# Performance work log

Measured on AMD Instinct MI355X. Metric: run time of the kernel, lower is better.

## Reference

```python
import jax, jax.numpy as jnp
import numpy as np

ATOM_F = 64
NBR_F = 64
IN_F = 2 * ATOM_F + NBR_F  # 192
ATTN = ATOM_F              # 64
ATTN_OUT = 4 * ATOM_F      # 256
EPS = 1e-5


def setup_inputs() -> dict:
    key = jax.random.key(0)
    ks = jax.random.split(key, 12)
    N, M = 65536, 12
    atom_in_fea = jax.random.normal(ks[0], (N, ATOM_F), dtype=jnp.float32)
    nbr_fea = jax.random.normal(ks[1], (N, M, NBR_F), dtype=jnp.float32)
    nbr_fea_idx = jax.random.randint(ks[2], (N, M), 0, N)
    s = 0.05
    WK = jax.random.normal(ks[3], (ATTN, IN_F), dtype=jnp.float32) * s
    WQ = jax.random.normal(ks[4], (ATTN, IN_F), dtype=jnp.float32) * s
    WV = jax.random.normal(ks[5], (ATTN, IN_F), dtype=jnp.float32) * s
    WO = jax.random.normal(ks[6], (ATTN_OUT, ATTN), dtype=jnp.float32) * s
    W_fc = jax.random.normal(ks[7], (2 * ATOM_F, ATTN_OUT), dtype=jnp.float32) * s
    b_fc = jax.random.normal(ks[8], (2 * ATOM_F,), dtype=jnp.float32) * s
    bn1_g = jnp.ones((2 * ATOM_F,), jnp.float32)
    bn1_b = jnp.zeros((2 * ATOM_F,), jnp.float32)
    bn2_g = jnp.ones((ATOM_F,), jnp.float32)
    bn2_b = jnp.zeros((ATOM_F,), jnp.float32)
    return {"atom_in_fea": atom_in_fea, "nbr_fea": nbr_fea, "nbr_fea_idx": nbr_fea_idx,
            "WK": WK, "WQ": WQ, "WV": WV, "WO": WO, "W_fc": W_fc, "b_fc": b_fc,
            "bn1_g": bn1_g, "bn1_b": bn1_b, "bn2_g": bn2_g, "bn2_b": bn2_b}


def _batchnorm(x2d, g, b):
    # training-mode BatchNorm1d: biased variance over the batch dim
    mean = jnp.mean(x2d, axis=0)
    var = jnp.mean((x2d - mean) ** 2, axis=0)
    return (x2d - mean) * jax.lax.rsqrt(var + EPS) * g + b


def reference(atom_in_fea, nbr_fea, nbr_fea_idx, WK, WQ, WV, WO,
              W_fc, b_fc, bn1_g, bn1_b, bn2_g, bn2_b):
    N, M = nbr_fea_idx.shape
    atom_nbr_fea = atom_in_fea[nbr_fea_idx]                       # (N, M, F)
    self_fea = jnp.broadcast_to(atom_in_fea[:, None, :], (N, M, ATOM_F))
    total = jnp.concatenate([self_fea, atom_nbr_fea, nbr_fea], axis=2)  # (N, M, 192)

    # self-attention over the M neighbor slots (dropout is identity at eval)
    K = jnp.einsum('nmf,af->nma', total, WK)
    Q = jnp.einsum('nmf,af->nma', total, WQ)
    V = jnp.einsum('nmf,af->nma', total, WV)
    logits = jnp.einsum('nma,nka->nmk', K, Q) / jnp.sqrt(jnp.float32(ATTN))
    w = jax.nn.softmax(logits, axis=-1)
    attn = jnp.einsum('nmk,nka->nma', w, V)                       # (N, M, 64)
    h = jnp.einsum('nma,oa->nmo', attn, WO)                       # (N, M, 256)

    gated = jnp.einsum('nmo,go->nmg', h, W_fc) + b_fc             # (N, M, 128)
    gated = _batchnorm(gated.reshape(-1, 2 * ATOM_F), bn1_g, bn1_b).reshape(N, M, 2 * ATOM_F)
    nbr_filter, nbr_core = jnp.split(gated, 2, axis=2)
    nbr_sumed = jnp.sum(jax.nn.sigmoid(nbr_filter) * jax.nn.softplus(nbr_core), axis=1)  # (N, 64)
    nbr_sumed = _batchnorm(nbr_sumed, bn2_g, bn2_b)
    return jax.nn.softplus(atom_in_fea + nbr_sumed)
```

## Files before the change

### kernel.cpp

```cpp
#include <hip/hip_runtime.h>
#include <stdint.h>


typedef unsigned short u16;
typedef __attribute__((ext_vector_type(8))) short short8;
typedef __attribute__((ext_vector_type(4))) short short4v;
typedef __attribute__((ext_vector_type(4))) float floatx4;

#define EPS 1e-5f
#define LOG2E 1.44269504f

#if defined(__has_builtin)
#if __has_builtin(__builtin_amdgcn_mfma_f32_16x16x16bf16_1k)
#define HAVE_M16 1
#endif
#if __has_builtin(__builtin_amdgcn_cvt_pk_bf16_f32)
#define HAVE_PK 1
#endif
#endif
#ifndef HAVE_M16
#define HAVE_M16 0
#endif
#ifndef HAVE_PK
#define HAVE_PK 0
#endif

#if HAVE_M16
#define VKW 20
#define WKW 20
#else
#define VKW 40
#define WKW 40
#endif

__device__ __forceinline__ u16 bf16r(float x) {
  uint32_t u = __float_as_uint(x);
  u = (u + 0x7fffu + ((u >> 16) & 1u)) >> 16;
  return (u16)u;
}
__device__ __forceinline__ float bf2f(u16 h) {
  return __uint_as_float(((uint32_t)h) << 16);
}
#if HAVE_PK
typedef __attribute__((ext_vector_type(2))) __bf16 bf16x2_t;
__device__ __forceinline__ uint32_t pkbf16(float a, float b) {
  bf16x2_t v = __builtin_amdgcn_cvt_pk_bf16_f32(a, b);
  return __builtin_bit_cast(uint32_t, v);
}
#else
__device__ __forceinline__ uint32_t pkbf16(float a, float b) {
  return (uint32_t)bf16r(a) | ((uint32_t)bf16r(b) << 16);
}
#endif
__device__ __forceinline__ short8 pkfrag(float4 a, float4 b) {
  union { uint32_t u[4]; short8 s; } r;
  r.u[0] = pkbf16(a.x, a.y); r.u[1] = pkbf16(a.z, a.w);
  r.u[2] = pkbf16(b.x, b.y); r.u[3] = pkbf16(b.z, b.w);
  return r.s;
}
__device__ __forceinline__ float fexp(float x) { return __builtin_amdgcn_exp2f(x * LOG2E); }
__device__ __forceinline__ float frcp(float x) { return __builtin_amdgcn_rcpf(x); }
__device__ __forceinline__ float fsig(float x) { return frcp(1.0f + fexp(-x)); }
__device__ __forceinline__ float fsp(float x) {
  return fmaxf(x, 0.0f) + __builtin_amdgcn_logf(1.0f + fexp(-fabsf(x))) * 0.69314718f;
}

#define MFMA32(a, b, c) __builtin_amdgcn_mfma_f32_16x16x32_bf16((a), (b), (c), 0, 0, 0)

#define OFF_FRAGE 0
#define OFF_FRAGP 24576
#define OFF_FRAGC 73728
#define OFF_BN1S1 90112
#define OFF_BN1S2 221184
#define OFF_BN2S1 352256
#define OFF_BN2S2 417792
#define OFF_BNST  483328
#define OFF_NSUM  524288
#define OFF_P     17825792
#define OFF_ATTN  68157440

__global__ __launch_bounds__(256) void k_prep(
    const float* __restrict__ WK, const float* __restrict__ WQ, const float* __restrict__ WV,
    const float* __restrict__ WO, const float* __restrict__ Wfc,
    u16* __restrict__ fragE, u16* __restrict__ fragP, u16* __restrict__ fragC,
    float* __restrict__ zbase) {
  int b = blockIdx.x, t = threadIdx.x;
  if (b < 24) {
    int c = b >> 1, ks = b & 1;
    for (int e = t; e < 512; e += 256) {
      int l = e >> 3, j = e & 7;
      int col = c * 16 + (l & 15);
      int k = ks * 32 + ((l >> 4) & 3) * 8 + j;
      int which = col >> 6, a = col & 63;
      const float* W = (which == 0) ? WK : ((which == 1) ? WQ : WV);
      fragE[b * 512 + e] = bf16r(W[a * 192 + 128 + k]);
    }
  } else if (b < 72) {
    int tt = b - 24; int ks = tt & 1; int ct = tt >> 1;
    int part = ct / 12; int rem = ct % 12; int which = rem >> 2; int a16 = rem & 3;
    for (int e = t; e < 512; e += 256) {
      int l = e >> 3, j = e & 7;
      int a = a16 * 16 + (l & 15);
      int k = ks * 32 + ((l >> 4) & 3) * 8 + j;
      const float* W = (which == 0) ? WK : ((which == 1) ? WQ : WV);
      fragP[tt * 512 + e] = bf16r(W[a * 192 + part * 64 + k]);
    }
  } else if (b < 88) {
    int tile = b - 72;
    for (int e = t; e < 512; e += 256) {
      int l = e >> 3, j = e & 7;
      int g = (tile >> 1) * 16 + (l & 15);
      int a = (tile & 1) * 32 + ((l >> 4) & 3) * 8 + j;
      float acc = 0.f;
#pragma unroll 8
      for (int o = 0; o < 256; ++o) acc += Wfc[g * 256 + o] * WO[o * 64 + a];
      fragC[tile * 512 + e] = bf16r(acc);
    }
  } else {
    int idx = (b - 88) * 256 + t;
    if (idx < 98304) zbase[idx] = 0.f;
  }
}

__global__ __launch_bounds__(256) void k_proj(
    const float* __restrict__ atom_in, const u16* __restrict__ fragP,
    u16* __restrict__ P, int N) {
  int tid = threadIdx.x, lane = tid & 63, wid = tid >> 6;
  int rowbase = (blockIdx.x * 4 + wid) * 16;
  __shared__ __align__(16) u16 aA[4][16][72];
  for (int rr = 0; rr < 16; ++rr)
    aA[wid][rr][lane] = bf16r(atom_in[(size_t)(rowbase + rr) * 64 + lane]);
  int cl = lane & 15, q = lane >> 4;
  short8 a0 = *(const short8*)&aA[wid][cl][q * 8];
  short8 a1 = *(const short8*)&aA[wid][cl][32 + q * 8];
  for (int tile = 0; tile < 24; ++tile) {
    floatx4 acc = {0.f, 0.f, 0.f, 0.f};
    short8 b0 = *(const short8*)(fragP + (tile * 2 + 0) * 512 + lane * 8);
    short8 b1 = *(const short8*)(fragP + (tile * 2 + 1) * 512 + lane * 8);
    acc = MFMA32(a0, b0, acc);
    acc = MFMA32(a1, b1, acc);
    int part = tile / 12, rem = tile % 12;
    int which = rem >> 2, a16 = rem & 3;
    u16* Pm = P + (size_t)(part * 3 + which) * N * 64;
    int colb = a16 * 16 + cl;
    for (int r = 0; r < 4; ++r) {
      int nrow = rowbase + q * 4 + r;
      Pm[(size_t)nrow * 64 + colb] = bf16r(acc[r]);
    }
  }
}

__global__ __launch_bounds__(256, 6) void k_main(
    const float* __restrict__ nbr_fea, const int* __restrict__ nbr_idx,
    const u16* __restrict__ P, const u16* __restrict__ fragE,
    const u16* __restrict__ fragC, const float* __restrict__ b_fc,
    u16* __restrict__ attn_out, float* __restrict__ bn1s1, float* __restrict__ bn1s2,
    int N) {
  int tid = threadIdx.x, lane = tid & 63, wid = tid >> 6;
  int n = blockIdx.x * 4 + wid;
  int cl = lane & 15, q = lane >> 4;

  __shared__ __align__(16) u16 KQ[4][16][72];
  __shared__ __align__(16) u16 Vt[4][64][VKW];
  union WU { u16 w[16][WKW]; float red[2][128]; };
  __shared__ __align__(16) WU WR[4];

#if HAVE_M16
  *(uint32_t*)&Vt[wid][lane][12] = 0u;
  *(uint32_t*)&Vt[wid][lane][14] = 0u;
#else
#pragma unroll
  for (int kk = 12; kk < 32; kk += 2) *(uint32_t*)&Vt[wid][lane][kk] = 0u;
#endif

  short8 ea0, ea1;
  if (cl < 12) {
    const float* rp = nbr_fea + ((size_t)n * 12 + cl) * 64 + q * 8;
    float4 a0 = *(const float4*)rp;
    float4 a1 = *(const float4*)(rp + 4);
    float4 b0 = *(const float4*)(rp + 32);
    float4 b1 = *(const float4*)(rp + 36);
    ea0 = pkfrag(a0, a1);
    ea1 = pkfrag(b0, b1);
  } else {
#pragma unroll
    for (int j = 0; j < 8; ++j) { ea0[j] = 0; ea1[j] = 0; }
  }

  int gv[4];
#pragma unroll
  for (int r = 0; r < 4; ++r) {
    int row = q * 4 + r;
    gv[r] = (row < 12) ? nbr_idx[n * 12 + row] : 0;
  }

#define STAGE1_TILE(c, which)                                                 \
  {                                                                           \
    floatx4 acc = {0.f, 0.f, 0.f, 0.f};                                       \
    short8 b0 = *(const short8*)(fragE + ((c) * 2 + 0) * 512 + lane * 8);     \
    short8 b1 = *(const short8*)(fragE + ((c) * 2 + 1) * 512 + lane * 8);     \
    acc = MFMA32(ea0, b0, acc);                                               \
    acc = MFMA32(ea1, b1, acc);                                               \
    int colb = ((c) & 3) * 16 + cl;                                           \
    float ps = bf2f(P[(size_t)(which) * N * 64 + (size_t)n * 64 + colb]);     \
    const u16* Pn = P + (size_t)(3 + (which)) * N * 64;                       \
    float v0 = acc[0] + ps + bf2f(Pn[(size_t)gv[0] * 64 + colb]);             \
    float v1 = acc[1] + ps + bf2f(Pn[(size_t)gv[1] * 64 + colb]);             \
    float v2 = acc[2] + ps + bf2f(Pn[(size_t)gv[2] * 64 + colb]);             \
    float v3 = acc[3] + ps + bf2f(Pn[(size_t)gv[3] * 64 + colb]);             \
    uint32_t p01 = pkbf16(v0, v1), p23 = pkbf16(v2, v3);                      \
    if ((which) < 2) {                                                        \
      KQ[wid][q * 4 + 0][colb] = (u16)p01;                                    \
      KQ[wid][q * 4 + 1][colb] = (u16)(p01 >> 16);                            \
      KQ[wid][q * 4 + 2][colb] = (u16)p23;                                    \
      KQ[wid][q * 4 + 3][colb] = (u16)(p23 >> 16);                            \
    } else if (q < 3) {                                                       \
      *(uint2*)&Vt[wid][colb][q * 4] = make_uint2(p01, p23);                  \
    }                                                                         \
  }

#pragma unroll
  for (int c = 0; c < 4; ++c) STAGE1_TILE(c, 0)
  short8 ka0 = *(const short8*)&KQ[wid][cl][q * 8];
  short8 ka1 = *(const short8*)&KQ[wid][cl][32 + q * 8];
#pragma unroll
  for (int c = 4; c < 8; ++c) STAGE1_TILE(c, 1)
  short8 qb0 = *(const short8*)&KQ[wid][cl][q * 8];
  short8 qb1 = *(const short8*)&KQ[wid][cl][32 + q * 8];
#pragma unroll
  for (int c = 8; c < 12; ++c) STAGE1_TILE(c, 2)

  floatx4 lacc = {0.f, 0.f, 0.f, 0.f};
  lacc = MFMA32(ka0, qb0, lacc);
  lacc = MFMA32(ka1, qb1, lacc);

  float w4[4];
#pragma unroll
  for (int r = 0; r < 4; ++r) {
    float x = lacc[r] * 0.125f;
    float mx = (cl < 12) ? x : -3.0e38f;
    mx = fmaxf(mx, __shfl_xor(mx, 1));
    mx = fmaxf(mx, __shfl_xor(mx, 2));
    mx = fmaxf(mx, __shfl_xor(mx, 4));
    mx = fmaxf(mx, __shfl_xor(mx, 8));
    float e = (cl < 12) ? fexp(x - mx) : 0.f;
    float s = e;
    s += __shfl_xor(s, 1); s += __shfl_xor(s, 2);
    s += __shfl_xor(s, 4); s += __shfl_xor(s, 8);
    w4[r] = e * frcp(s);
  }
  {
    uint32_t p01 = pkbf16(w4[0], w4[1]), p23 = pkbf16(w4[2], w4[3]);
    WR[wid].w[q * 4 + 0][cl] = (u16)p01;
    WR[wid].w[q * 4 + 1][cl] = (u16)(p01 >> 16);
    WR[wid].w[q * 4 + 2][cl] = (u16)p23;
    WR[wid].w[q * 4 + 3][cl] = (u16)(p23 >> 16);
  }
#if !HAVE_M16
  for (int i = lane; i < 128; i += 64) {
    int rr = i >> 3, cc = 16 + ((i & 7) << 1);
    *(uint32_t*)&WR[wid].w[rr][cc] = 0u;
  }
#endif

#if HAVE_M16
  short4v wa = *(const short4v*)&WR[wid].w[cl][q * 4];
#pragma unroll
  for (int c = 0; c < 4; ++c) {
    floatx4 acc = {0.f, 0.f, 0.f, 0.f};
    short4v vb = *(const short4v*)&Vt[wid][c * 16 + cl][q * 4];
    acc = __builtin_amdgcn_mfma_f32_16x16x16bf16_1k(wa, vb, acc, 0, 0, 0);
    uint32_t p01 = pkbf16(acc[0], acc[1]), p23 = pkbf16(acc[2], acc[3]);
    KQ[wid][q * 4 + 0][c * 16 + cl] = (u16)p01;
    KQ[wid][q * 4 + 1][c * 16 + cl] = (u16)(p01 >> 16);
    KQ[wid][q * 4 + 2][c * 16 + cl] = (u16)p23;
    KQ[wid][q * 4 + 3][c * 16 + cl] = (u16)(p23 >> 16);
  }
#else
  short8 wa = *(const short8*)&WR[wid].w[cl][q * 8];
#pragma unroll
  for (int c = 0; c < 4; ++c) {
    floatx4 acc = {0.f, 0.f, 0.f, 0.f};
    short8 vb = *(const short8*)&Vt[wid][c * 16 + cl][q * 8];
    acc = MFMA32(wa, vb, acc);
    uint32_t p01 = pkbf16(acc[0], acc[1]), p23 = pkbf16(acc[2], acc[3]);
    KQ[wid][q * 4 + 0][c * 16 + cl] = (u16)p01;
    KQ[wid][q * 4 + 1][c * 16 + cl] = (u16)(p01 >> 16);
    KQ[wid][q * 4 + 2][c * 16 + cl] = (u16)p23;
    KQ[wid][q * 4 + 3][c * 16 + cl] = (u16)(p23 >> 16);
  }
#endif

#pragma unroll
  for (int i = 0; i < 3; ++i) {
    int j = i * 64 + lane;
    uint2 d = *(const uint2*)&KQ[wid][j >> 4][(j & 15) * 4];
    *(uint2*)(attn_out + ((size_t)n * 12 + (j >> 4)) * 64 + (j & 15) * 4) = d;
  }

  short8 aa0 = *(const short8*)&KQ[wid][cl][q * 8];
  short8 aa1 = *(const short8*)&KQ[wid][cl][32 + q * 8];
  float regA[8], regB[8];
#pragma unroll
  for (int c = 0; c < 8; ++c) {
    floatx4 acc = {0.f, 0.f, 0.f, 0.f};
    short8 b0 = *(const short8*)(fragC + (c * 2 + 0) * 512 + lane * 8);
    short8 b1 = *(const short8*)(fragC + (c * 2 + 1) * 512 + lane * 8);
    acc = MFMA32(aa0, b0, acc);
    acc = MFMA32(aa1, b1, acc);
    float bias = b_fc[c * 16 + cl];
    float s1 = 0.f, s2 = 0.f;
    if (q < 3) {
#pragma unroll
      for (int r = 0; r < 4; ++r) {
        float v = acc[r] + bias;
        s1 += v; s2 += v * v;
      }
    }
    s1 += __shfl_xor(s1, 16); s1 += __shfl_xor(s1, 32);
    s2 += __shfl_xor(s2, 16); s2 += __shfl_xor(s2, 32);
    regA[c] = s1; regB[c] = s2;
  }
  if (lane < 16) {
#pragma unroll
    for (int c = 0; c < 8; ++c) {
      WR[wid].red[0][c * 16 + cl] = regA[c];
      WR[wid].red[1][c * 16 + cl] = regB[c];
    }
  }
  __syncthreads();
  if (tid < 128) {
    float a1 = WR[0].red[0][tid] + WR[1].red[0][tid] + WR[2].red[0][tid] + WR[3].red[0][tid];
    float a2 = WR[0].red[1][tid] + WR[1].red[1][tid] + WR[2].red[1][tid] + WR[3].red[1][tid];
    int rep = blockIdx.x & 255;
    atomicAdd(&bn1s1[rep * 128 + tid], a1);
    atomicAdd(&bn1s2[rep * 128 + tid], a2);
  }
}

__global__ __launch_bounds__(256) void k_bn1(
    const float* __restrict__ bn1s1, const float* __restrict__ bn1s2,
    const float* __restrict__ g1, const float* __restrict__ b1,
    const float* __restrict__ bfc, float* __restrict__ bnst, float count) {
  int t = threadIdx.x;
  int f = t & 127, half = t >> 7;
  float s1 = 0.f, s2 = 0.f;
  for (int r = half * 128; r < half * 128 + 128; ++r) {
    s1 += bn1s1[r * 128 + f]; s2 += bn1s2[r * 128 + f];
  }
  __shared__ float p1[256], p2[256];
  p1[t] = s1; p2[t] = s2;
  __syncthreads();
  if (t < 128) {
    s1 = p1[t] + p1[t + 128]; s2 = p2[t] + p2[t + 128];
    float mean = s1 / count;
    float var = s2 / count - mean * mean;
    float sc = g1[t] * rsqrtf(var + EPS);
    bnst[t] = sc;
    bnst[128 + t] = (bfc[t] - mean) * sc + b1[t];
  }
}

__global__ __launch_bounds__(256) void k_gate(
    const u16* __restrict__ attn, const u16* __restrict__ fragC,
    const float* __restrict__ bnst,
    float* __restrict__ ns, float* __restrict__ bn2s1, float* __restrict__ bn2s2, int N) {
  int tid = threadIdx.x, lane = tid & 63, wid = tid >> 6;
  int n = blockIdx.x * 4 + wid;
  int cl = lane & 15, q = lane >> 4;
  __shared__ float scS[128], shS[128];
  __shared__ float r1[4][64], r2[4][64];
  if (tid < 128) scS[tid] = bnst[tid];
  else           shS[tid - 128] = bnst[tid];
  __syncthreads();

  short8 aa0, aa1;
  if (cl < 12) {
    const u16* rp = attn + ((size_t)n * 12 + cl) * 64;
    aa0 = *(const short8*)(rp + q * 8);
    aa1 = *(const short8*)(rp + 32 + q * 8);
  } else {
#pragma unroll
    for (int j = 0; j < 8; ++j) { aa0[j] = 0; aa1[j] = 0; }
  }

  floatx4 acc[8];
#pragma unroll
  for (int c = 0; c < 8; ++c) {
    floatx4 z = {0.f, 0.f, 0.f, 0.f};
    short8 b0 = *(const short8*)(fragC + (c * 2 + 0) * 512 + lane * 8);
    short8 b1 = *(const short8*)(fragC + (c * 2 + 1) * 512 + lane * 8);
    z = MFMA32(aa0, b0, z);
    acc[c] = MFMA32(aa1, b1, z);
  }

  float s[4];
#pragma unroll
  for (int c = 0; c < 4; ++c) {
    int gF = c * 16 + cl, gC = gF + 64;
    float scf = scS[gF], shf = shS[gF], scc = scS[gC], shc = shS[gC];
    float sum = 0.f;
    if (q < 3) {
#pragma unroll
      for (int r = 0; r < 4; ++r) {
        float xf = acc[c][r] * scf + shf;
        float xc = acc[c + 4][r] * scc + shc;
        sum += fsig(xf) * fsp(xc);
      }
    }
    sum += __shfl_xor(sum, 16);
    sum += __shfl_xor(sum, 32);
    s[c] = sum;
  }
  if (lane < 16) {
#pragma unroll
    for (int c = 0; c < 4; ++c) {
      ns[(size_t)n * 64 + c * 16 + cl] = s[c];
      r1[wid][c * 16 + cl] = s[c];
      r2[wid][c * 16 + cl] = s[c] * s[c];
    }
  }
  __syncthreads();
  if (tid < 64) {
    float a1 = r1[0][tid] + r1[1][tid] + r1[2][tid] + r1[3][tid];
    float a2 = r2[0][tid] + r2[1][tid] + r2[2][tid] + r2[3][tid];
    int rep = blockIdx.x & 255;
    atomicAdd(&bn2s1[rep * 64 + tid], a1);
    atomicAdd(&bn2s2[rep * 64 + tid], a2);
  }
}

__global__ __launch_bounds__(256) void k_bn2(
    const float* __restrict__ bn2s1, const float* __restrict__ bn2s2,
    const float* __restrict__ g2, const float* __restrict__ b2,
    float* __restrict__ bnst, float count) {
  int t = threadIdx.x;
  int f = t & 63, part = t >> 6;
  float s1 = 0.f, s2 = 0.f;
  for (int r = part * 64; r < part * 64 + 64; ++r) {
    s1 += bn2s1[r * 64 + f]; s2 += bn2s2[r * 64 + f];
  }
  __shared__ float p1[256], p2[256];
  p1[t] = s1; p2[t] = s2;
  __syncthreads();
  if (t < 64) {
    s1 = p1[t] + p1[t + 64] + p1[t + 128] + p1[t + 192];
    s2 = p2[t] + p2[t + 64] + p2[t + 128] + p2[t + 192];
    float mean = s1 / count;
    float var = s2 / count - mean * mean;
    float sc = g2[t] * rsqrtf(var + EPS);
    bnst[256 + t] = sc;
    bnst[320 + t] = b2[t] - mean * sc;
  }
}

__global__ __launch_bounds__(256) void k_out(
    const float* __restrict__ atom_in, const float* __restrict__ ns,
    const float* __restrict__ bnst, float* __restrict__ out, int total) {
  int i = blockIdx.x * 256 + threadIdx.x;
  if (i < total) {
    int f = i & 63;
    float v = atom_in[i] + ns[i] * bnst[256 + f] + bnst[320 + f];
    out[i] = fsp(v);
  }
}

extern "C" void kernel_launch(void* const* d_in, const int* in_sizes, int n_in,
                              void* d_out, int out_size, void* d_ws, size_t ws_size,
                              hipStream_t stream) {
  const float* atom_in = (const float*)d_in[0];
  const float* nbr_fea = (const float*)d_in[1];
  const int*   nbr_idx = (const int*)d_in[2];
  const float* WK  = (const float*)d_in[3];
  const float* WQ  = (const float*)d_in[4];
  const float* WV  = (const float*)d_in[5];
  const float* WO  = (const float*)d_in[6];
  const float* Wfc = (const float*)d_in[7];
  const float* bfc = (const float*)d_in[8];
  const float* g1  = (const float*)d_in[9];
  const float* b1  = (const float*)d_in[10];
  const float* g2  = (const float*)d_in[11];
  const float* b2  = (const float*)d_in[12];
  int N = in_sizes[0] / 64;

  char* ws = (char*)d_ws;
  u16*   fragE = (u16*)(ws + OFF_FRAGE);
  u16*   fragP = (u16*)(ws + OFF_FRAGP);
  u16*   fragC = (u16*)(ws + OFF_FRAGC);
  float* bn1s1 = (float*)(ws + OFF_BN1S1);
  float* bn1s2 = (float*)(ws + OFF_BN1S2);
  float* bn2s1 = (float*)(ws + OFF_BN2S1);
  float* bn2s2 = (float*)(ws + OFF_BN2S2);
  float* bnst  = (float*)(ws + OFF_BNST);
  float* nsum  = (float*)(ws + OFF_NSUM);
  u16*   P     = (u16*)(ws + OFF_P);
  u16*   attn  = (u16*)(ws + OFF_ATTN);
  float* out   = (float*)d_out;

  hipLaunchKernelGGL(k_prep, dim3(472), dim3(256), 0, stream,
                     WK, WQ, WV, WO, Wfc, fragE, fragP, fragC, bn1s1);
  hipLaunchKernelGGL(k_proj, dim3(N / 64), dim3(256), 0, stream, atom_in, fragP, P, N);
  hipLaunchKernelGGL(k_main, dim3(N / 4), dim3(256), 0, stream,
                     nbr_fea, nbr_idx, P, fragE, fragC, bfc, attn, bn1s1, bn1s2, N);
  hipLaunchKernelGGL(k_bn1, dim3(1), dim3(256), 0, stream,
                     bn1s1, bn1s2, g1, b1, bfc, bnst, (float)(N * 12));
  hipLaunchKernelGGL(k_gate, dim3(N / 4), dim3(256), 0, stream,
                     attn, fragC, bnst, nsum, bn2s1, bn2s2, N);
  hipLaunchKernelGGL(k_bn2, dim3(1), dim3(256), 0, stream,
                     bn2s1, bn2s2, g2, b2, bnst, (float)N);
  hipLaunchKernelGGL(k_out, dim3((N * 64) / 256), dim3(256), 0, stream,
                     atom_in, nsum, bnst, out, N * 64);
}
```

Before: 624.5 us.

## Interleave projection table for vectorized gathers, drop softmax max, widen BN reductions

The per-atom projection table P is re-laid out so the K/Q/V parts for one atom sit together, with each lane's four columns contiguous. k_main can then fetch self and neighbor projections with a few 8-byte loads issued up front instead of many scalar 2-byte gathers inside each tile. Neighbor indices are read as one int4, and occupancy bounds drop from 6 to 5 to make room for the prefetched registers. The softmax no longer subtracts the row max, which saves shuffles but can overflow for large logits. The single-block BN reduction kernels also use more threads.

```diff
diff --git a/kernel.cpp b/kernel.cpp
--- a/kernel.cpp
+++ b/kernel.cpp
@@ -141,16 +141,15 @@
     acc = MFMA32(a1, b1, acc);
     int part = tile / 12, rem = tile % 12;
     int which = rem >> 2, a16 = rem & 3;
-    u16* Pm = P + (size_t)(part * 3 + which) * N * 64;
-    int colb = a16 * 16 + cl;
+    u16* Pm = P + (size_t)part * N * 192;
     for (int r = 0; r < 4; ++r) {
       int nrow = rowbase + q * 4 + r;
-      Pm[(size_t)nrow * 64 + colb] = bf16r(acc[r]);
-    }
-  }
-}
-
-__global__ __launch_bounds__(256, 6) void k_main(
+      Pm[((size_t)nrow * 3 + which) * 64 + cl * 4 + a16] = bf16r(acc[r]);
+    }
+  }
+}
+
+__global__ __launch_bounds__(256, 5) void k_main(
     const float* __restrict__ nbr_fea, const int* __restrict__ nbr_idx,
     const u16* __restrict__ P, const u16* __restrict__ fragE,
     const u16* __restrict__ fragC, const float* __restrict__ b_fc,
@@ -165,13 +164,8 @@
   union WU { u16 w[16][WKW]; float red[2][128]; };
   __shared__ __align__(16) WU WR[4];
 
-#if HAVE_M16
-  *(uint32_t*)&Vt[wid][lane][12] = 0u;
-  *(uint32_t*)&Vt[wid][lane][14] = 0u;
-#else
-#pragma unroll
-  for (int kk = 12; kk < 32; kk += 2) *(uint32_t*)&Vt[wid][lane][kk] = 0u;
-#endif
+  int4 gi = *(const int4*)(nbr_idx + (size_t)n * 12 + (q < 3 ? q : 2) * 4);
+  int gv[4] = {gi.x, gi.y, gi.z, gi.w};
 
   short8 ea0, ea1;
   if (cl < 12) {
@@ -187,12 +181,24 @@
     for (int j = 0; j < 8; ++j) { ea0[j] = 0; ea1[j] = 0; }
   }
 
-  int gv[4];
-#pragma unroll
-  for (int r = 0; r < 4; ++r) {
-    int row = q * 4 + r;
-    gv[r] = (row < 12) ? nbr_idx[n * 12 + row] : 0;
-  }
+  const u16* Pnb = P + (size_t)N * 192;
+  uint2 sW[3], nW[3][4];
+#pragma unroll
+  for (int w = 0; w < 3; ++w)
+    sW[w] = *(const uint2*)(P + ((size_t)n * 3 + w) * 64 + cl * 4);
+#pragma unroll
+  for (int w = 0; w < 3; ++w)
+#pragma unroll
+    for (int r = 0; r < 4; ++r)
+      nW[w][r] = *(const uint2*)(Pnb + ((size_t)gv[r] * 3 + w) * 64 + cl * 4);
+
+#if HAVE_M16
+  *(uint32_t*)&Vt[wid][lane][12] = 0u;
+  *(uint32_t*)&Vt[wid][lane][14] = 0u;
+#else
+#pragma unroll
+  for (int kk = 12; kk < 32; kk += 2) *(uint32_t*)&Vt[wid][lane][kk] = 0u;
+#endif
 
 #define STAGE1_TILE(c, which)                                                 \
   {                                                                           \
@@ -202,12 +208,12 @@
     acc = MFMA32(ea0, b0, acc);                                               \
     acc = MFMA32(ea1, b1, acc);                                               \
     int colb = ((c) & 3) * 16 + cl;                                           \
-    float ps = bf2f(P[(size_t)(which) * N * 64 + (size_t)n * 64 + colb]);     \
-    const u16* Pn = P + (size_t)(3 + (which)) * N * 64;                       \
-    float v0 = acc[0] + ps + bf2f(Pn[(size_t)gv[0] * 64 + colb]);             \
-    float v1 = acc[1] + ps + bf2f(Pn[(size_t)gv[1] * 64 + colb]);             \
-    float v2 = acc[2] + ps + bf2f(Pn[(size_t)gv[2] * 64 + colb]);             \
-    float v3 = acc[3] + ps + bf2f(Pn[(size_t)gv[3] * 64 + colb]);             \
+    const u16* sp = (const u16*)&sW[(which)];                                 \
+    float ps = bf2f(sp[(c) & 3]);                                             \
+    float v0 = acc[0] + ps + bf2f(((const u16*)&nW[(which)][0])[(c) & 3]);    \
+    float v1 = acc[1] + ps + bf2f(((const u16*)&nW[(which)][1])[(c) & 3]);    \
+    float v2 = acc[2] + ps + bf2f(((const u16*)&nW[(which)][2])[(c) & 3]);    \
+    float v3 = acc[3] + ps + bf2f(((const u16*)&nW[(which)][3])[(c) & 3]);    \
     uint32_t p01 = pkbf16(v0, v1), p23 = pkbf16(v2, v3);                      \
     if ((which) < 2) {                                                        \
       KQ[wid][q * 4 + 0][colb] = (u16)p01;                                    \
@@ -237,13 +243,7 @@
   float w4[4];
 #pragma unroll
   for (int r = 0; r < 4; ++r) {
-    float x = lacc[r] * 0.125f;
-    float mx = (cl < 12) ? x : -3.0e38f;
-    mx = fmaxf(mx, __shfl_xor(mx, 1));
-    mx = fmaxf(mx, __shfl_xor(mx, 2));
-    mx = fmaxf(mx, __shfl_xor(mx, 4));
-    mx = fmaxf(mx, __shfl_xor(mx, 8));
-    float e = (cl < 12) ? fexp(x - mx) : 0.f;
+    float e = (cl < 12) ? fexp(lacc[r] * 0.125f) : 0.f;
     float s = e;
     s += __shfl_xor(s, 1); s += __shfl_xor(s, 2);
     s += __shfl_xor(s, 4); s += __shfl_xor(s, 8);
@@ -338,21 +338,23 @@
   }
 }
 
-__global__ __launch_bounds__(256) void k_bn1(
+__global__ __launch_bounds__(1024) void k_bn1(
     const float* __restrict__ bn1s1, const float* __restrict__ bn1s2,
     const float* __restrict__ g1, const float* __restrict__ b1,
     const float* __restrict__ bfc, float* __restrict__ bnst, float count) {
   int t = threadIdx.x;
-  int f = t & 127, half = t >> 7;
+  int f = t & 127, chunk = t >> 7;
   float s1 = 0.f, s2 = 0.f;
-  for (int r = half * 128; r < half * 128 + 128; ++r) {
+  for (int r = chunk * 32; r < chunk * 32 + 32; ++r) {
     s1 += bn1s1[r * 128 + f]; s2 += bn1s2[r * 128 + f];
   }
-  __shared__ float p1[256], p2[256];
+  __shared__ float p1[1024], p2[1024];
   p1[t] = s1; p2[t] = s2;
   __syncthreads();
   if (t < 128) {
-    s1 = p1[t] + p1[t + 128]; s2 = p2[t] + p2[t + 128];
+    s1 = 0.f; s2 = 0.f;
+#pragma unroll
+    for (int k = 0; k < 8; ++k) { s1 += p1[t + 128 * k]; s2 += p2[t + 128 * k]; }
     float mean = s1 / count;
     float var = s2 / count - mean * mean;
     float sc = g1[t] * rsqrtf(var + EPS);
@@ -430,22 +432,23 @@
   }
 }
 
-__global__ __launch_bounds__(256) void k_bn2(
+__global__ __launch_bounds__(512) void k_bn2(
     const float* __restrict__ bn2s1, const float* __restrict__ bn2s2,
     const float* __restrict__ g2, const float* __restrict__ b2,
     float* __restrict__ bnst, float count) {
   int t = threadIdx.x;
   int f = t & 63, part = t >> 6;
   float s1 = 0.f, s2 = 0.f;
-  for (int r = part * 64; r < part * 64 + 64; ++r) {
+  for (int r = part * 32; r < part * 32 + 32; ++r) {
     s1 += bn2s1[r * 64 + f]; s2 += bn2s2[r * 64 + f];
   }
-  __shared__ float p1[256], p2[256];
+  __shared__ float p1[512], p2[512];
   p1[t] = s1; p2[t] = s2;
   __syncthreads();
   if (t < 64) {
-    s1 = p1[t] + p1[t + 64] + p1[t + 128] + p1[t + 192];
-    s2 = p2[t] + p2[t + 64] + p2[t + 128] + p2[t + 192];
+    s1 = 0.f; s2 = 0.f;
+#pragma unroll
+    for (int k = 0; k < 8; ++k) { s1 += p1[t + 64 * k]; s2 += p2[t + 64 * k]; }
     float mean = s1 / count;
     float var = s2 / count - mean * mean;
     float sc = g2[t] * rsqrtf(var + EPS);
@@ -502,11 +505,11 @@
   hipLaunchKernelGGL(k_proj, dim3(N / 64), dim3(256), 0, stream, atom_in, fragP, P, N);
   hipLaunchKernelGGL(k_main, dim3(N / 4), dim3(256), 0, stream,
                      nbr_fea, nbr_idx, P, fragE, fragC, bfc, attn, bn1s1, bn1s2, N);
-  hipLaunchKernelGGL(k_bn1, dim3(1), dim3(256), 0, stream,
+  hipLaunchKernelGGL(k_bn1, dim3(1), dim3(1024), 0, stream,
                      bn1s1, bn1s2, g1, b1, bfc, bnst, (float)(N * 12));
   hipLaunchKernelGGL(k_gate, dim3(N / 4), dim3(256), 0, stream,
                      attn, fragC, bnst, nsum, bn2s1, bn2s2, N);
-  hipLaunchKernelGGL(k_bn2, dim3(1), dim3(256), 0, stream,
+  hipLaunchKernelGGL(k_bn2, dim3(1), dim3(512), 0, stream,
                      bn2s1, bn2s2, g2, b2, bnst, (float)N);
   hipLaunchKernelGGL(k_out, dim3((N * 64) / 256), dim3(256), 0, stream,
                      atom_in, nsum, bnst, out, N * 64);
```

Result: faster. 572.2 us (-8.4%).
